# Kernel tuning notes

Measured on AMD Instinct MI355X. Metric: run time of the kernel, lower is better.

Reference implementation:

```python
import jax, jax.numpy as jnp
import numpy as np

T, B, H, W, C = 7, 4, 96, 96, 256
NH, KD = 8, 32  # num_heads, key_dim (attention_filters)


def setup_inputs() -> dict:
    key = jax.random.key(0)
    ks = jax.random.split(key, 8)
    s = 0.02
    return {
        "frames": jax.random.normal(ks[0], (T, B, H, W, C), jnp.float32),
        "t_emb": jax.random.normal(ks[1], (T, C), jnp.float32) * s,  # Embedding(T, C)
        "Wq": jax.random.normal(ks[2], (C, NH, KD), jnp.float32) * s,
        "bq": jnp.zeros((NH, KD), jnp.float32),
        "Wk": jax.random.normal(ks[3], (C, NH, KD), jnp.float32) * s,
        "bk": jnp.zeros((NH, KD), jnp.float32),
        "Wv": jax.random.normal(ks[4], (C, NH, KD), jnp.float32) * s,
        "bv": jnp.zeros((NH, KD), jnp.float32),
        "Wo": jax.random.normal(ks[5], (NH, KD, C), jnp.float32) * s,
        "bo": jnp.zeros((C,), jnp.float32),
    }


def reference(frames, t_emb, Wq, bq, Wk, bk, Wv, bv, Wo, bo):
    # frames: (T, B, H, W, C). Temporal embedding added to keys and queries,
    # values are raw frames. Attention is over the T axis independently at each
    # (b, h, w) location. query_idx defaults to all T frames, so all T single-
    # query MHA calls are batched into one attention with Tq = T.
    emb = t_emb[:, None, None, None, :]            # (T,1,1,1,C)
    kq_in = frames + emb                            # keys and queries share this
    q = jnp.einsum('qbhwc,cnd->qbhwnd', kq_in, Wq) + bq
    k = jnp.einsum('tbhwc,cnd->tbhwnd', kq_in, Wk) + bk
    v = jnp.einsum('tbhwc,cnd->tbhwnd', frames, Wv) + bv
    scale = 1.0 / jnp.sqrt(jnp.asarray(KD, q.dtype))
    scores = jnp.einsum('qbhwnd,tbhwnd->bhwnqt', q, k) * scale  # (B,H,W,NH,Tq,Tk)
    attn = jax.nn.softmax(scores, axis=-1)
    ctx = jnp.einsum('bhwnqt,tbhwnd->qbhwnd', attn, v)
    out = jnp.einsum('qbhwnd,ndc->qbhwc', ctx, Wo) + bo  # (T,B,H,W,C)
    return out
```

## Files before the change

kernel.cpp:

```cpp
#include <hip/hip_runtime.h>
#include <stdint.h>

#define TT 7
#define CC 256
#define NPOSC 36864

typedef unsigned int uint;
typedef unsigned short ushort_t;
typedef __attribute__((ext_vector_type(8))) short short8;
typedef __attribute__((ext_vector_type(4))) float f32x4;

__device__ inline float bf2f(ushort_t u) {
    union { uint i; float f; } v; v.i = ((uint)u) << 16; return v.f;
}
__device__ inline ushort_t f2bf(float f) {
    union { float f; uint i; } v; v.f = f;
    uint i = v.i;
    return (ushort_t)((i + 0x7FFFu + ((i >> 16) & 1u)) >> 16);
}
__device__ inline uint pack2(float a, float b) {
    return (uint)f2bf(a) | (((uint)f2bf(b)) << 16);
}
__device__ inline short8 as_s8(uint4 v) {
    union { uint4 u; short8 s; } x; x.u = v; return x.s;
}

__global__ void prep_kernel(const float* __restrict__ Wq, const float* __restrict__ Wk,
                            const float* __restrict__ Wv, const float* __restrict__ Wo,
                            const float* __restrict__ bq, const float* __restrict__ bk,
                            const float* __restrict__ bv, const float* __restrict__ temb,
                            ushort_t* __restrict__ WTall, ushort_t* __restrict__ WoT,
                            float* __restrict__ biasC)
{
    int bx = blockIdx.x, tid = threadIdx.x;
    if (bx < 64) {
        __shared__ __align__(16) ushort_t tl[64][72];
        int m = bx >> 4, tile = bx & 15;
        int tr = (tile >> 2) * 64, tc = (tile & 3) * 64;
        const float* src = (m == 0) ? Wq : (m == 1) ? Wk : (m == 2) ? Wv : Wo;
        ushort_t* dst = (m < 3) ? (WTall + m * 65536) : WoT;
        int lr = tid >> 2, lc = (tid & 3) * 16;
        const float* sp = src + (size_t)(tr + lr) * 256 + tc + lc;
        #pragma unroll
        for (int q = 0; q < 4; ++q) {
            float4 x = *(const float4*)(sp + q * 4);
            tl[lr][lc + q * 4 + 0] = f2bf(x.x);
            tl[lr][lc + q * 4 + 1] = f2bf(x.y);
            tl[lr][lc + q * 4 + 2] = f2bf(x.z);
            tl[lr][lc + q * 4 + 3] = f2bf(x.w);
        }
        __syncthreads();
        uint w[8];
        #pragma unroll
        for (int j = 0; j < 8; ++j) {
            ushort_t e0 = tl[lc + 2 * j][lr];
            ushort_t e1 = tl[lc + 2 * j + 1][lr];
            w[j] = (uint)e0 | ((uint)e1 << 16);
        }
        uint4 o0, o1;
        o0.x = w[0]; o0.y = w[1]; o0.z = w[2]; o0.w = w[3];
        o1.x = w[4]; o1.y = w[5]; o1.z = w[6]; o1.w = w[7];
        *(uint4*)(dst + (size_t)(tc + lr) * 256 + tr + lc) = o0;
        *(uint4*)(dst + (size_t)(tc + lr) * 256 + tr + lc + 8) = o1;
    } else {
        int gid = (bx - 64) * 256 + tid;
        int t = gid / 768, j = gid % 768;
        float val;
        if (j < 256) {
            val = bq[j];
        } else if (j < 512) {
            val = bk[j - 256];
        } else {
            int nd = j - 512;
            float acc = bv[nd];
            for (int c = 0; c < 256; ++c)
                acc -= temb[t * 256 + c] * Wv[(size_t)c * 256 + nd];
            val = acc;
        }
        biasC[t * 768 + j] = val;
    }
}

__launch_bounds__(256, 2)
__global__ void qkv_kernel(const float* __restrict__ frames, const float* __restrict__ temb,
                           const ushort_t* __restrict__ WTall, const float* __restrict__ biasC,
                           ushort_t* __restrict__ qkvT, int posBase, int Ps)
{
    int t = blockIdx.y;
    int pos0l = blockIdx.x * 128;
    int tid = threadIdx.x;
    int wave = tid >> 6, lane = tid & 63;
    int mh = wave >> 1, nh = wave & 1;
    int l15 = lane & 15, lg = lane >> 4;

    __shared__ __align__(16) ushort_t Atile[2][64][40];

    uint4 Breg[4][8];
    {
        const float* fb = frames + ((size_t)t * NPOSC + posBase + pos0l + nh * 64) * 256;
        #pragma unroll
        for (int kc = 0; kc < 8; ++kc) {
            float4 e0 = *(const float4*)(temb + t * 256 + kc * 32 + lg * 8);
            float4 e1 = *(const float4*)(temb + t * 256 + kc * 32 + lg * 8 + 4);
            #pragma unroll
            for (int nt = 0; nt < 4; ++nt) {
                const float* xp = fb + (size_t)(nt * 16 + l15) * 256 + kc * 32 + lg * 8;
                float4 x0 = *(const float4*)(xp);
                float4 x1 = *(const float4*)(xp + 4);
                uint4 r;
                r.x = pack2(x0.x + e0.x, x0.y + e0.y);
                r.y = pack2(x0.z + e0.z, x0.w + e0.w);
                r.z = pack2(x1.x + e1.x, x1.y + e1.y);
                r.w = pack2(x1.z + e1.z, x1.w + e1.w);
                Breg[nt][kc] = r;
            }
        }
    }

    f32x4 acc[2][4];
    const f32x4 z4 = {0.f, 0.f, 0.f, 0.f};
    #pragma unroll
    for (int mt = 0; mt < 2; ++mt)
        #pragma unroll
        for (int nt = 0; nt < 4; ++nt) acc[mt][nt] = z4;

    int srow = tid >> 2, sq4 = tid & 3;

    {
        uint4 sv = *(const uint4*)(WTall + (size_t)srow * 256 + sq4 * 8);
        *(uint4*)&Atile[0][srow][sq4 * 8] = sv;
    }

    for (int ndc = 0; ndc < 12; ++ndc) {
        #pragma unroll
        for (int kc = 0; kc < 8; ++kc) {
            int it = ndc * 8 + kc;
            int buf = kc & 1;
            uint4 nxt;
            bool have = (it + 1 < 96);
            if (have) {
                int it1 = it + 1;
                nxt = *(const uint4*)(WTall + ((size_t)((it1 >> 3) * 64 + srow)) * 256
                                      + (it1 & 7) * 32 + sq4 * 8);
            }
            __syncthreads();
            if (have) *(uint4*)&Atile[buf ^ 1][srow][sq4 * 8] = nxt;

            uint4 af[2];
            #pragma unroll
            for (int mt = 0; mt < 2; ++mt)
                af[mt] = *(const uint4*)&Atile[buf][mh * 32 + mt * 16 + l15][lg * 8];
            #pragma unroll
            for (int mt = 0; mt < 2; ++mt)
                #pragma unroll
                for (int nt = 0; nt < 4; ++nt)
                    acc[mt][nt] = __builtin_amdgcn_mfma_f32_16x16x32_bf16(
                        as_s8(af[mt]), as_s8(Breg[nt][kc]), acc[mt][nt], 0, 0, 0);
        }
        #pragma unroll
        for (int mt = 0; mt < 2; ++mt) {
            int ndbase = ndc * 64 + mh * 32 + mt * 16 + lg * 4;
            float bi[4];
            #pragma unroll
            for (int i = 0; i < 4; ++i) bi[i] = biasC[t * 768 + ndbase + i];
            #pragma unroll
            for (int nt = 0; nt < 4; ++nt) {
                int posl = pos0l + nh * 64 + nt * 16 + l15;
                #pragma unroll
                for (int i = 0; i < 4; ++i) {
                    float v = acc[mt][nt][i] + bi[i];
                    qkvT[((size_t)(ndbase + i) * 7 + t) * Ps + posl] = f2bf(v);
                }
                acc[mt][nt] = z4;
            }
        }
    }
}

__global__ void attn_kernel(const ushort_t* __restrict__ qkvT, ushort_t* __restrict__ ctxT, int Ps)
{
    int n = blockIdx.y;
    int pos = blockIdx.x * 256 + threadIdx.x;
    const float scale = 0.17677669529663687f;
    float s[7][7];
    #pragma unroll
    for (int a = 0; a < 7; ++a)
        #pragma unroll
        for (int b = 0; b < 7; ++b) s[a][b] = 0.f;

    const ushort_t* qp = qkvT + ((size_t)(n * 32) * 7) * Ps + pos;
    const ushort_t* kp = qkvT + ((size_t)(256 + n * 32) * 7) * Ps + pos;

    for (int d = 0; d < 32; ++d) {
        float qv[7], kv[7];
        #pragma unroll
        for (int i = 0; i < 7; ++i) qv[i] = bf2f(qp[(size_t)(d * 7 + i) * Ps]);
        #pragma unroll
        for (int i = 0; i < 7; ++i) kv[i] = bf2f(kp[(size_t)(d * 7 + i) * Ps]);
        #pragma unroll
        for (int a = 0; a < 7; ++a)
            #pragma unroll
            for (int b = 0; b < 7; ++b) s[a][b] += qv[a] * kv[b];
    }

    #pragma unroll
    for (int a = 0; a < 7; ++a) {
        float mx = -1e30f;
        #pragma unroll
        for (int b = 0; b < 7; ++b) { s[a][b] *= scale; mx = fmaxf(mx, s[a][b]); }
        float sum = 0.f;
        #pragma unroll
        for (int b = 0; b < 7; ++b) {
            float e = exp2f((s[a][b] - mx) * 1.4426950408889634f);
            s[a][b] = e; sum += e;
        }
        float r = 1.0f / sum;
        #pragma unroll
        for (int b = 0; b < 7; ++b) s[a][b] *= r;
    }

    const ushort_t* vp = qkvT + ((size_t)(512 + n * 32) * 7) * Ps + pos;
    const size_t K7P = (size_t)7 * Ps;
    ushort_t* cb = ctxT + (size_t)(n * 32) * K7P + pos;

    #pragma unroll
    for (int dc = 0; dc < 4; ++dc) {
        float o[7][8];
        #pragma unroll
        for (int a = 0; a < 7; ++a)
            #pragma unroll
            for (int j = 0; j < 8; ++j) o[a][j] = 0.f;
        #pragma unroll
        for (int kt = 0; kt < 7; ++kt) {
            float vv[8];
            #pragma unroll
            for (int j = 0; j < 8; ++j)
                vv[j] = bf2f(vp[(size_t)((dc * 8 + j) * 7 + kt) * Ps]);
            #pragma unroll
            for (int a = 0; a < 7; ++a)
                #pragma unroll
                for (int j = 0; j < 8; ++j) o[a][j] += s[a][kt] * vv[j];
        }
        #pragma unroll
        for (int j = 0; j < 8; ++j) {
            ushort_t* cj = cb + (size_t)(dc * 8 + j) * K7P;
            #pragma unroll
            for (int a = 0; a < 7; ++a)
                cj[(size_t)a * Ps] = f2bf(o[a][j]);
        }
    }
}

__launch_bounds__(256, 2)
__global__ void out_kernel(const ushort_t* __restrict__ ctxT, const ushort_t* __restrict__ WoT,
                           const float* __restrict__ bo, float* __restrict__ outp,
                           int posBase, int Ps)
{
    int rows0 = blockIdx.x * 128;
    int c0 = blockIdx.y * 128;
    int tid = threadIdx.x, wave = tid >> 6, lane = tid & 63;
    int mh = wave >> 1, nh = wave & 1;
    int l15 = lane & 15, lg = lane >> 4;
    const size_t K7P = (size_t)7 * Ps;

    __shared__ __align__(16) ushort_t At[2][128][40];
    __shared__ __align__(16) ushort_t Bt[2][128][40];

    int ndl = tid >> 3;
    int rg  = tid & 7;
    int csw = ((((ndl >> 3) ^ (rg & 3)) << 3) | (ndl & 7));

    f32x4 acc[4][4];
    const f32x4 z4 = {0.f, 0.f, 0.f, 0.f};
    #pragma unroll
    for (int mt = 0; mt < 4; ++mt)
        #pragma unroll
        for (int nt = 0; nt < 4; ++nt) acc[mt][nt] = z4;

    {
        const ushort_t* ap = ctxT + (size_t)ndl * K7P + rows0 + rg * 8;
        union { uint4 u; ushort_t s[8]; } ua, ub;
        ua.u = *(const uint4*)ap;
        ub.u = *(const uint4*)(ap + 64);
        #pragma unroll
        for (int i = 0; i < 8; ++i) {
            At[0][rg * 8 + i][csw] = ua.s[i];
            At[0][64 + rg * 8 + i][csw] = ub.s[i];
        }
        #pragma unroll
        for (int p = 0; p < 2; ++p) {
            int ch = p * 256 + tid, row = ch >> 2, q4 = ch & 3;
            uint4 bv_ = *(const uint4*)(WoT + (size_t)(c0 + row) * 256 + q4 * 8);
            *(uint4*)&Bt[0][row][q4 * 8] = bv_;
        }
    }

    #pragma unroll
    for (int kc = 0; kc < 8; ++kc) {
        int buf = kc & 1;
        uint4 na0, na1, nb[2];
        if (kc < 7) {
            const ushort_t* ap = ctxT + (size_t)((kc + 1) * 32 + ndl) * K7P + rows0 + rg * 8;
            na0 = *(const uint4*)ap;
            na1 = *(const uint4*)(ap + 64);
            #pragma unroll
            for (int p = 0; p < 2; ++p) {
                int ch = p * 256 + tid, row = ch >> 2, q4 = ch & 3;
                nb[p] = *(const uint4*)(WoT + (size_t)(c0 + row) * 256 + (kc + 1) * 32 + q4 * 8);
            }
        }
        __syncthreads();
        if (kc < 7) {
            union { uint4 u; ushort_t s[8]; } ua, ub;
            ua.u = na0; ub.u = na1;
            #pragma unroll
            for (int i = 0; i < 8; ++i) {
                At[buf ^ 1][rg * 8 + i][csw] = ua.s[i];
                At[buf ^ 1][64 + rg * 8 + i][csw] = ub.s[i];
            }
            #pragma unroll
            for (int p = 0; p < 2; ++p) {
                int ch = p * 256 + tid, row = ch >> 2, q4 = ch & 3;
                *(uint4*)&Bt[buf ^ 1][row][q4 * 8] = nb[p];
            }
        }
        uint4 af[4], bfr[4];
        #pragma unroll
        for (int mt = 0; mt < 4; ++mt) {
            int r = mh * 64 + mt * 16 + l15;
            af[mt] = *(const uint4*)&At[buf][r][(lg ^ ((r >> 3) & 3)) << 3];
        }
        #pragma unroll
        for (int nt = 0; nt < 4; ++nt)
            bfr[nt] = *(const uint4*)&Bt[buf][nh * 64 + nt * 16 + l15][lg * 8];
        #pragma unroll
        for (int mt = 0; mt < 4; ++mt)
            #pragma unroll
            for (int nt = 0; nt < 4; ++nt)
                acc[mt][nt] = __builtin_amdgcn_mfma_f32_16x16x32_bf16(
                    as_s8(af[mt]), as_s8(bfr[nt]), acc[mt][nt], 0, 0, 0);
    }

    int t = rows0 / Ps;
    int prow = rows0 - t * Ps;
    size_t obase = (size_t)t * NPOSC + posBase + prow;
    #pragma unroll
    for (int nt = 0; nt < 4; ++nt) {
        int col = c0 + nh * 64 + nt * 16 + l15;
        float bov = bo[col];
        #pragma unroll
        for (int mt = 0; mt < 4; ++mt) {
            #pragma unroll
            for (int i = 0; i < 4; ++i) {
                int r = mh * 64 + mt * 16 + lg * 4 + i;
                outp[(obase + r) * 256 + col] = acc[mt][nt][i] + bov;
            }
        }
    }
}

extern "C" void kernel_launch(void* const* d_in, const int* in_sizes, int n_in,
                              void* d_out, int out_size, void* d_ws, size_t ws_size,
                              hipStream_t stream)
{
    const float* frames = (const float*)d_in[0];
    const float* temb   = (const float*)d_in[1];
    const float* Wq = (const float*)d_in[2];
    const float* bq = (const float*)d_in[3];
    const float* Wk = (const float*)d_in[4];
    const float* bk = (const float*)d_in[5];
    const float* Wv = (const float*)d_in[6];
    const float* bv = (const float*)d_in[7];
    const float* Wo = (const float*)d_in[8];
    const float* bo = (const float*)d_in[9];
    float* outp = (float*)d_out;

    char* w = (char*)d_ws;
    ushort_t* WTall = (ushort_t*)w;
    ushort_t* WoT   = (ushort_t*)(w + 393216);
    float*    biasC = (float*)(w + 524288);
    const size_t fixed = 557056;

    int s = 1;
    for (; s < 16; s *= 2) {
        size_t Ps_ = (size_t)NPOSC / s;
        size_t need = fixed + 768ull * 7 * Ps_ * 2 + 7ull * Ps_ * 256 * 2;
        if (need <= ws_size) break;
    }
    int Ps = NPOSC / s;
    ushort_t* qkvT = (ushort_t*)(w + fixed);
    ushort_t* ctxp = (ushort_t*)(w + fixed + (size_t)768 * 7 * Ps * 2);

    prep_kernel<<<85, 256, 0, stream>>>(Wq, Wk, Wv, Wo, bq, bk, bv, temb,
                                        WTall, WoT, biasC);
    for (int sl = 0; sl < s; ++sl) {
        int posBase = sl * Ps;
        qkv_kernel<<<dim3(Ps / 128, 7), 256, 0, stream>>>(frames, temb, WTall, biasC,
                                                          qkvT, posBase, Ps);
        attn_kernel<<<dim3(Ps / 256, 8), 256, 0, stream>>>(qkvT, ctxp, Ps);
        out_kernel<<<dim3(7 * Ps / 128, 2), 256, 0, stream>>>(ctxp, WoT, bo, outp,
                                                              posBase, Ps);
    }
}
```

Measured before the change: 902.9 us.

## Stage full weight chunks into LDS via direct global-to-LDS loads with XOR swizzle

After: 858.2 us. 5.0% less time.

```diff
diff --git a/kernel.cpp b/kernel.cpp
--- a/kernel.cpp
+++ b/kernel.cpp
@@ -60,8 +60,11 @@
         uint4 o0, o1;
         o0.x = w[0]; o0.y = w[1]; o0.z = w[2]; o0.w = w[3];
         o1.x = w[4]; o1.y = w[5]; o1.z = w[6]; o1.w = w[7];
-        *(uint4*)(dst + (size_t)(tc + lr) * 256 + tr + lc) = o0;
-        *(uint4*)(dst + (size_t)(tc + lr) * 256 + tr + lc + 8) = o1;
+        int row = tc + lr;
+        int sw = (m < 3) ? ((row & 7) << 3) : 0;
+        int c0u = tr + lc;
+        *(uint4*)(dst + (size_t)row * 256 + (c0u ^ sw)) = o0;
+        *(uint4*)(dst + (size_t)row * 256 + ((c0u + 8) ^ sw)) = o1;
     } else {
         int gid = (bx - 64) * 256 + tid;
         int t = gid / 768, j = gid % 768;
@@ -83,7 +86,7 @@
 
 __launch_bounds__(256, 2)
 __global__ void qkv_kernel(const float* __restrict__ frames, const float* __restrict__ temb,
-                           const ushort_t* __restrict__ WTall, const float* __restrict__ biasC,
+                           const ushort_t* __restrict__ WTsw, const float* __restrict__ biasC,
                            ushort_t* __restrict__ qkvT, int posBase, int Ps)
 {
     int t = blockIdx.y;
@@ -93,7 +96,7 @@
     int mh = wave >> 1, nh = wave & 1;
     int l15 = lane & 15, lg = lane >> 4;
 
-    __shared__ __align__(16) ushort_t Atile[2][64][40];
+    __shared__ __align__(16) ushort_t Atile[2][64][256];
 
     uint4 Breg[4][8];
     {
@@ -124,32 +127,36 @@
         #pragma unroll
         for (int nt = 0; nt < 4; ++nt) acc[mt][nt] = z4;
 
-    int srow = tid >> 2, sq4 = tid & 3;
-
-    {
-        uint4 sv = *(const uint4*)(WTall + (size_t)srow * 256 + sq4 * 8);
-        *(uint4*)&Atile[0][srow][sq4 * 8] = sv;
-    }
+    const char* wsrc = (const char*)WTsw + (size_t)(wave * 8) * 1024 + (size_t)lane * 16;
+    char* lbase = (char*)&Atile[0][0][0] + (size_t)(wave * 8) * 1024;
+
+    #pragma unroll
+    for (int i = 0; i < 8; ++i)
+        __builtin_amdgcn_global_load_lds(
+            (const __attribute__((address_space(1))) void*)(wsrc + i * 1024),
+            (__attribute__((address_space(3))) void*)(lbase + i * 1024), 16, 0, 0);
+    __syncthreads();
 
     for (int ndc = 0; ndc < 12; ++ndc) {
+        int buf = ndc & 1;
+        if (ndc < 11) {
+            const char* src = wsrc + (size_t)(ndc + 1) * 32768;
+            char* nb = lbase + (size_t)(buf ^ 1) * 32768;
+            #pragma unroll
+            for (int i = 0; i < 8; ++i)
+                __builtin_amdgcn_global_load_lds(
+                    (const __attribute__((address_space(1))) void*)(src + i * 1024),
+                    (__attribute__((address_space(3))) void*)(nb + i * 1024), 16, 0, 0);
+        }
         #pragma unroll
         for (int kc = 0; kc < 8; ++kc) {
-            int it = ndc * 8 + kc;
-            int buf = kc & 1;
-            uint4 nxt;
-            bool have = (it + 1 < 96);
-            if (have) {
-                int it1 = it + 1;
-                nxt = *(const uint4*)(WTall + ((size_t)((it1 >> 3) * 64 + srow)) * 256
-                                      + (it1 & 7) * 32 + sq4 * 8);
-            }
-            __syncthreads();
-            if (have) *(uint4*)&Atile[buf ^ 1][srow][sq4 * 8] = nxt;
-
             uint4 af[2];
             #pragma unroll
-            for (int mt = 0; mt < 2; ++mt)
-                af[mt] = *(const uint4*)&Atile[buf][mh * 32 + mt * 16 + l15][lg * 8];
+            for (int mt = 0; mt < 2; ++mt) {
+                int r = mh * 32 + mt * 16 + l15;
+                int colb = (kc * 64 + lg * 16) ^ ((r & 7) << 4);
+                af[mt] = *(const uint4*)((const char*)&Atile[buf][r][0] + colb);
+            }
             #pragma unroll
             for (int mt = 0; mt < 2; ++mt)
                 #pragma unroll
@@ -174,6 +181,7 @@
                 acc[mt][nt] = z4;
             }
         }
+        __syncthreads();
     }
 }
 
```
